# Optimization experiments

Hardware: AMD Instinct MI355X
Metric: run time of the kernel (lower is better)

The kernel has to match this reference:

```python
import jax, jax.numpy as jnp
import numpy as np

K = 3        # kernel size
PAD = 1      # padding
DG = 16      # deformable groups
MAXR = 10.0  # max_residue_magnitude


def _lrelu(x):
    return jnp.where(x >= 0, x, 0.1 * x)


def _conv3(x, w, b):
    y = jax.lax.conv_general_dilated(x, w, (1, 1), 'SAME',
                                     dimension_numbers=('NCHW', 'OIHW', 'NCHW'))
    return y + b[None, :, None, None]


def _deform_conv2d(x, offset, mask, weight, bias):
    # x: [B,Cin,H,W]; offset: [B,2*DG*K*K,H,W]; mask: [B,DG*K*K,H,W]
    B, Cin, H, W = x.shape
    Cout = weight.shape[0]
    G, Cg, K2 = DG, Cin // DG, K * K
    off = offset.reshape(B, G, K2, 2, H, W)
    dy, dx = off[:, :, :, 0], off[:, :, :, 1]
    ky = jnp.repeat(jnp.arange(K), K).astype(x.dtype)   # [K2]
    kx = jnp.tile(jnp.arange(K), K).astype(x.dtype)
    hh = jnp.arange(H, dtype=x.dtype)
    ww = jnp.arange(W, dtype=x.dtype)
    # sampling positions [B,G,K2,H,W]
    py = dy + ky[None, None, :, None, None] + hh[None, None, None, :, None] - PAD
    px = dx + kx[None, None, :, None, None] + ww[None, None, None, None, :] - PAD
    y0 = jnp.floor(py)
    x0 = jnp.floor(px)
    wy1 = py - y0
    wx1 = px - x0
    xf = x.reshape(B, G, Cg, H * W)

    def gather(yi, xi, wgt):
        valid = (yi >= 0) & (yi <= H - 1) & (xi >= 0) & (xi <= W - 1)
        idx = (jnp.clip(yi, 0, H - 1).astype(jnp.int32) * W
               + jnp.clip(xi, 0, W - 1).astype(jnp.int32)).reshape(B, G, -1)
        vals = jnp.take_along_axis(
            xf, jnp.broadcast_to(idx[:, :, None, :], (B, G, Cg, idx.shape[-1])), axis=3)
        vals = vals.reshape(B, G, Cg, K2, H, W)
        w = (wgt * valid.astype(x.dtype))[:, :, None]  # [B,G,1,K2,H,W]
        return vals * w

    s = (gather(y0, x0, (1 - wy1) * (1 - wx1))
         + gather(y0, x0 + 1, (1 - wy1) * wx1)
         + gather(y0 + 1, x0, wy1 * (1 - wx1))
         + gather(y0 + 1, x0 + 1, wy1 * wx1))
    s = s * mask.reshape(B, G, K2, H, W)[:, :, None]
    wr = weight.reshape(Cout, G, Cg, K2)
    out = jnp.einsum('ogck,bgckhw->bohw', wr, s)
    return out + bias[None, :, None, None]


def setup_inputs() -> dict:
    key = jax.random.key(0)
    ks = jax.random.split(key, 16)
    B, Cin, Cout, H, W = 4, 128, 64, 96, 96
    Coff = 3 * Cout + 4  # 196
    stdv = 1.0 / np.sqrt(Cin * K * K)
    inp = {
        'x': jax.random.normal(ks[0], (B, Cin, H, W), jnp.float32),
        'extra_feat': jax.random.normal(ks[1], (B, 3 * Cout, H, W), jnp.float32),
        'flow_1': jax.random.normal(ks[2], (B, 2, H, W), jnp.float32),
        'flow_2': jax.random.normal(ks[3], (B, 2, H, W), jnp.float32),
        'weight': jax.random.uniform(ks[4], (Cout, Cin, K, K), jnp.float32, -stdv, stdv),
        'bias': jax.random.normal(ks[5], (Cout,), jnp.float32) * 0.01,
        'ow0': jax.random.normal(ks[6], (Cout, Coff, K, K), jnp.float32) * 0.02,
        'ob0': jnp.zeros((Cout,), jnp.float32),
        'ow1': jax.random.normal(ks[7], (Cout, Cout, K, K), jnp.float32) * 0.02,
        'ob1': jnp.zeros((Cout,), jnp.float32),
        'ow2': jax.random.normal(ks[8], (Cout, Cout, K, K), jnp.float32) * 0.02,
        'ob2': jnp.zeros((Cout,), jnp.float32),
        'ow3': jax.random.normal(ks[9], (27 * DG, Cout, K, K), jnp.float32) * 0.01,
        'ob3': jnp.zeros((27 * DG,), jnp.float32),
    }
    return inp


def reference(x, extra_feat, flow_1, flow_2, weight, bias,
              ow0, ob0, ow1, ob1, ow2, ob2, ow3, ob3):
    feat = jnp.concatenate([extra_feat, flow_1, flow_2], axis=1)
    h = _lrelu(_conv3(feat, ow0, ob0))
    h = _lrelu(_conv3(h, ow1, ob1))
    h = _lrelu(_conv3(h, ow2, ob2))
    out = _conv3(h, ow3, ob3)
    o1, o2, m = jnp.split(out, 3, axis=1)
    offs = MAXR * jnp.tanh(jnp.concatenate([o1, o2], axis=1))
    off1, off2 = jnp.split(offs, 2, axis=1)
    off1 = off1 + jnp.tile(flow_1[:, ::-1], (1, off1.shape[1] // 2, 1, 1))
    off2 = off2 + jnp.tile(flow_2[:, ::-1], (1, off2.shape[1] // 2, 1, 1))
    offset = jnp.concatenate([off1, off2], axis=1)
    mask = jax.nn.sigmoid(m)
    return _deform_conv2d(x, offset, mask, weight, bias)
```

## Files before the change

### kernel.cpp

```cpp
#include <hip/hip_runtime.h>
#include <math.h>

#define HW 9216
#define Hh 96
#define Ww 96
#define PHW 9604

typedef __attribute__((ext_vector_type(8))) short bh8;
typedef __attribute__((ext_vector_type(4))) short bh4;
typedef __attribute__((ext_vector_type(4))) float f32x4;
typedef __attribute__((ext_vector_type(2))) float f32x2;
typedef __attribute__((ext_vector_type(4))) int i32x4;
union bh8i { bh8 v; i32x4 i; };

__device__ __forceinline__ short f2bf(float f) {
    union { float f; unsigned u; } v; v.f = f;
    unsigned r = v.u + 0x7FFFu + ((v.u >> 16) & 1u);
    return (short)(r >> 16);
}
__device__ __forceinline__ float bf2f(short s) {
    union { unsigned u; float f; } v; v.u = ((unsigned)(unsigned short)s) << 16;
    return v.f;
}
__device__ __forceinline__ float lo_bf(unsigned u) {
    union { unsigned u; float f; } v; v.u = u << 16; return v.f;
}
__device__ __forceinline__ float hi_bf(unsigned u) {
    union { unsigned u; float f; } v; v.u = u & 0xFFFF0000u; return v.f;
}
__device__ __forceinline__ int cvt_pk_bf16(float lo, float hi) {
    int r;
    asm("v_cvt_pk_bf16_f32 %0, %1, %2" : "=v"(r) : "v"(lo), "v"(hi));
    return r;
}

__global__ void prep_misc(short* __restrict__ xpad1, short* __restrict__ hpa,
                          short* __restrict__ hpb, short* __restrict__ xdp,
                          const float* __restrict__ ow0, const float* __restrict__ ow1,
                          const float* __restrict__ ow2, const float* __restrict__ ow3,
                          const float* __restrict__ wd,
                          short* __restrict__ wb0, short* __restrict__ wb1,
                          short* __restrict__ wb2, short* __restrict__ wb3,
                          short* __restrict__ wbd) {
    int i = blockIdx.x * 256 + threadIdx.x;
    const int z1 = 4 * 388 * 224, z2 = 4 * 388 * 64;
    if (i < z1 + 2 * z2) {
        short* p; int C;
        if (i < z1) { p = xpad1; C = 224; }
        else if (i < z1 + z2) { p = hpa; C = 64; i -= z1; }
        else { p = hpb; C = 64; i -= z1 + z2; }
        int c = i % C;
        int r = i / C;
        int b = r / 388, pid = r - b * 388;
        int row, col;
        if (pid < 98)       { row = 0;  col = pid; }
        else if (pid < 196) { row = 97; col = pid - 98; }
        else if (pid < 292) { row = pid - 196 + 1; col = 0; }
        else                { row = pid - 292 + 1; col = 97; }
        p[((size_t)b * PHW + row * 98 + col) * C + c] = 0;
        return;
    }
    i -= z1 + 2 * z2;
    const int zr = 4 * 16 * 388 * 8;
    if (i < zr) {
        int c8 = i & 7;
        int r = i >> 3;
        int pid = r % 388;
        int bg = r / 388;
        int row, col;
        if (pid < 98)       { row = 0;  col = pid; }
        else if (pid < 196) { row = 97; col = pid - 98; }
        else if (pid < 292) { row = pid - 196 + 1; col = 0; }
        else                { row = pid - 292 + 1; col = 97; }
        xdp[((size_t)bg * PHW + row * 98 + col) * 8 + c8] = 0;
        return;
    }
    i -= zr;
    const int n0 = 64 * 9 * 224, n1 = 64 * 9 * 64, n3 = 448 * 9 * 64, nd = 64 * 1152;
    if (i < n0) {
        int co = i / (9 * 224); int r = i - co * (9 * 224);
        int tap = r / 224, ci = r - tap * 224;
        wb0[i] = f2bf(ci < 196 ? ow0[(co * 196 + ci) * 9 + tap] : 0.f);
        return;
    }
    i -= n0;
    if (i < n1) {
        int co = i / (9 * 64); int r = i - co * (9 * 64);
        int tap = r / 64, ci = r - tap * 64;
        wb1[i] = f2bf(ow1[(co * 64 + ci) * 9 + tap]);
        return;
    }
    i -= n1;
    if (i < n1) {
        int co = i / (9 * 64); int r = i - co * (9 * 64);
        int tap = r / 64, ci = r - tap * 64;
        wb2[i] = f2bf(ow2[(co * 64 + ci) * 9 + tap]);
        return;
    }
    i -= n1;
    if (i < n3) {
        int co = i / (9 * 64); int r = i - co * (9 * 64);
        int tap = r / 64, ci = r - tap * 64;
        wb3[i] = f2bf(co < 432 ? ow3[(co * 64 + ci) * 9 + tap] : 0.f);
        return;
    }
    i -= n3;
    if (i < nd) {
        int slab = i >> 11, r = i & 2047;
        int co = r >> 5, k = r & 31;
        int gt = slab * 4 + (k >> 3), c8 = k & 7;
        int g = gt / 9, tap = gt - g * 9;
        wbd[i] = f2bf(wd[(co * 128 + g * 8 + c8) * 9 + tap]);
    }
}

__global__ void pack_all(const float* __restrict__ extra,
                         const float* __restrict__ f1,
                         const float* __restrict__ f2,
                         const float* __restrict__ x,
                         short* __restrict__ xp,
                         short* __restrict__ xdp) {
    __shared__ float t[32][33];
    const int tid = threadIdx.x, tx = tid & 31, ty = tid >> 5;
    const int pt = blockIdx.x, b = blockIdx.z;
    if (blockIdx.y < 7) {
        const int ct = blockIdx.y;
#pragma unroll
        for (int j = 0; j < 4; ++j) {
            int ch = ct * 32 + ty + j * 8;
            int p = pt * 32 + tx;
            float v = 0.f;
            if (ch < 192)      v = extra[(b * 192 + ch) * HW + p];
            else if (ch < 194) v = f1[(b * 2 + ch - 192) * HW + p];
            else if (ch < 196) v = f2[(b * 2 + ch - 194) * HW + p];
            t[ty + j * 8][tx] = v;
        }
        __syncthreads();
#pragma unroll
        for (int j = 0; j < 4; ++j) {
            int pr = ty + j * 8;
            int p = pt * 32 + pr;
            int r = p / 96, c = p - r * 96;
            xp[((size_t)b * PHW + (r + 1) * 98 + (c + 1)) * 224 + ct * 32 + tx] =
                f2bf(t[tx][pr]);
        }
    } else {
        const int ct = blockIdx.y - 7;
#pragma unroll
        for (int j = 0; j < 4; ++j) {
            int ch = ct * 32 + ty + j * 8;
            t[ty + j * 8][tx] = x[((size_t)b * 128 + ch) * HW + pt * 32 + tx];
        }
        __syncthreads();
        if (tid < 128) {
            int oct = tid >> 5, p = tid & 31;
            int g = ct * 4 + oct;
            int pix = pt * 32 + p;
            int r = pix / 96, c = pix - r * 96;
            bh8 v;
#pragma unroll
            for (int cc = 0; cc < 8; ++cc) v[cc] = f2bf(t[oct * 8 + cc][p]);
            *(bh8*)&xdp[(((size_t)b * 16 + g) * PHW + (r + 1) * 98 + (c + 1)) * 8] = v;
        }
    }
}

template<int CINP, int KCH>
__launch_bounds__(256)
__global__ void conv_mfma(const short* __restrict__ xp,
                          const short* __restrict__ wb,
                          const float* __restrict__ bias,
                          short* __restrict__ o1) {
    __shared__ __attribute__((aligned(16))) short smA[9 * 64 * 32];
    const int tid = threadIdx.x;
    const int lane = tid & 63, wv = tid >> 6;
    const int q = lane >> 4, l15 = lane & 15;
    const int b = blockIdx.y;
    const int pix0 = blockIdx.x * 64 + wv * 16;
    const int soh = pix0 / 96, sow = pix0 - (pix0 / 96) * 96;

    const short* bp = xp + ((size_t)b * PHW + soh * 98 + sow + l15) * CINP + q * 8;

    const int sco = tid >> 2, sqq = tid & 3;
    const short* wsrc = wb + (size_t)sco * (9 * CINP) + sqq * 8;

    f32x4 acc[4];
#pragma unroll
    for (int t = 0; t < 4; ++t) acc[t] = (f32x4){0.f, 0.f, 0.f, 0.f};

    for (int p = 0; p < KCH; ++p) {
        __syncthreads();
        bh8 wtmp[9];
#pragma unroll
        for (int tap = 0; tap < 9; ++tap)
            wtmp[tap] = *(const bh8*)(wsrc + tap * CINP + p * 32);
#pragma unroll
        for (int tap = 0; tap < 9; ++tap)
            *(bh8*)&smA[tap * 2048 + sco * 32 + sqq * 8] = wtmp[tap];
        __syncthreads();
#pragma unroll
        for (int tap = 0; tap < 9; ++tap) {
            const int ky = tap / 3, kx = tap - (tap / 3) * 3;
            bh8 bf = *(const bh8*)(bp + (ky * 98 + kx) * CINP + p * 32);
#pragma unroll
            for (int t = 0; t < 4; ++t) {
                bh8 af = *(const bh8*)&smA[tap * 2048 + (t * 16 + l15) * 32 + q * 8];
                acc[t] = __builtin_amdgcn_mfma_f32_16x16x32_bf16(af, bf, acc[t], 0, 0, 0);
            }
        }
    }

    size_t base = ((size_t)b * PHW + (soh + 1) * 98 + sow + l15 + 1) * 64;
#pragma unroll
    for (int t = 0; t < 4; ++t) {
        bh4 v4;
#pragma unroll
        for (int r = 0; r < 4; ++r) {
            int co = t * 16 + q * 4 + r;
            float v = acc[t][r] + bias[co];
            v = (v >= 0.f) ? v : 0.1f * v;
            v4[r] = f2bf(v);
        }
        *(bh4*)(o1 + base + t * 16 + q * 4) = v4;
    }
}

__launch_bounds__(256)
__global__ void conv4_mfma(const short* __restrict__ xp,
                           const short* __restrict__ wb,
                           const float* __restrict__ bias,
                           float* __restrict__ offp,
                           short* __restrict__ maskb,
                           const float* __restrict__ flow1,
                           const float* __restrict__ flow2) {
    __shared__ __attribute__((aligned(16))) short smA[9 * 64 * 32];
    const int tid = threadIdx.x;
    const int lane = tid & 63, wv = tid >> 6;
    const int q = lane >> 4, l15 = lane & 15;
    const int b = blockIdx.y;
    const int cob = blockIdx.z * 64;
    const int pix0 = blockIdx.x * 64 + wv * 16;
    const int soh = pix0 / 96, sow = pix0 - (pix0 / 96) * 96;

    const short* bp = xp + ((size_t)b * PHW + soh * 98 + sow + l15) * 64 + q * 8;

    const int sco = tid >> 2, sqq = tid & 3;
    const short* wsrc = wb + (size_t)(cob + sco) * 576 + sqq * 8;

    f32x4 acc[4];
#pragma unroll
    for (int t = 0; t < 4; ++t) acc[t] = (f32x4){0.f, 0.f, 0.f, 0.f};

    for (int p = 0; p < 2; ++p) {
        __syncthreads();
        bh8 wtmp[9];
#pragma unroll
        for (int tap = 0; tap < 9; ++tap)
            wtmp[tap] = *(const bh8*)(wsrc + tap * 64 + p * 32);
#pragma unroll
        for (int tap = 0; tap < 9; ++tap)
            *(bh8*)&smA[tap * 2048 + sco * 32 + sqq * 8] = wtmp[tap];
        __syncthreads();
#pragma unroll
        for (int tap = 0; tap < 9; ++tap) {
            const int ky = tap / 3, kx = tap - (tap / 3) * 3;
            bh8 bf = *(const bh8*)(bp + (ky * 98 + kx) * 64 + p * 32);
#pragma unroll
            for (int t = 0; t < 4; ++t) {
                bh8 af = *(const bh8*)&smA[tap * 2048 + (t * 16 + l15) * 32 + q * 8];
                acc[t] = __builtin_amdgcn_mfma_f32_16x16x32_bf16(af, bf, acc[t], 0, 0, 0);
            }
        }
    }

    const int pix = pix0 + l15;
#pragma unroll
    for (int t = 0; t < 4; ++t) {
        int cb0 = cob + t * 16 + q * 4;
        if (cb0 < 288) {
            const float* fl = (cb0 < 144) ? flow1 : flow2;
            float fe = fl[(b * 2 + 1) * HW + pix];
            float fo = fl[(b * 2) * HW + pix];
            float t0 = 10.f * tanhf(acc[t][0] + bias[cb0 + 0]) + fe;
            float t1 = 10.f * tanhf(acc[t][1] + bias[cb0 + 1]) + fo;
            float t2 = 10.f * tanhf(acc[t][2] + bias[cb0 + 2]) + fe;
            float t3 = 10.f * tanhf(acc[t][3] + bias[cb0 + 3]) + fo;
            size_t p0 = ((size_t)b * 144 + (cb0 >> 1)) * HW + pix;
            *(f32x2*)&offp[p0 * 2] = (f32x2){t0, t1};
            *(f32x2*)&offp[(p0 + HW) * 2] = (f32x2){t2, t3};
        } else {
#pragma unroll
            for (int r = 0; r < 4; ++r) {
                int chn = cb0 + r;
                if (chn < 432) {
                    float v = acc[t][r] + bias[chn];
                    maskb[((size_t)b * 144 + (chn - 288)) * HW + pix] =
                        f2bf(1.f / (1.f + expf(-v)));
                }
            }
        }
    }
}

#define BLEND_MFMA(C0, C1, C2, C3, WWv, CL)                                    \
    {                                                                          \
        const f32x2 W00 = (f32x2){(WWv)[0], (WWv)[0]};                         \
        const f32x2 W01 = (f32x2){(WWv)[1], (WWv)[1]};                         \
        const f32x2 W10 = (f32x2){(WWv)[2], (WWv)[2]};                         \
        const f32x2 W11 = (f32x2){(WWv)[3], (WWv)[3]};                         \
        bh8i bf;                                                               \
        _Pragma("unroll")                                                      \
        for (int k = 0; k < 4; ++k) {                                          \
            unsigned u00 = (unsigned)(C0).i[k], u01 = (unsigned)(C1).i[k];     \
            unsigned u10 = (unsigned)(C2).i[k], u11 = (unsigned)(C3).i[k];     \
            f32x2 p00 = (f32x2){lo_bf(u00), hi_bf(u00)};                       \
            f32x2 p01 = (f32x2){lo_bf(u01), hi_bf(u01)};                       \
            f32x2 p10 = (f32x2){lo_bf(u10), hi_bf(u10)};                       \
            f32x2 p11 = (f32x2){lo_bf(u11), hi_bf(u11)};                       \
            f32x2 s = p00 * W00 + p01 * W01 + p10 * W10 + p11 * W11;           \
            bf.i[k] = cvt_pk_bf16(s[0], s[1]);                                 \
        }                                                                      \
        _Pragma("unroll")                                                      \
        for (int t = 0; t < 4; ++t) {                                          \
            bh8 af = *(const bh8*)&smW[(CL) * 2048 + (t * 16 + l15) * 32 + q * 8]; \
            acc[t] = __builtin_amdgcn_mfma_f32_16x16x32_bf16(af, bf.v, acc[t], 0, 0, 0); \
        }                                                                      \
    }

__launch_bounds__(256)
__global__ void deform_mfma(const short* __restrict__ xdp,
                            const float* __restrict__ offp,
                            const short* __restrict__ maskb,
                            const short* __restrict__ wbd,
                            const float* __restrict__ bias,
                            float* __restrict__ out) {
    __shared__ __attribute__((aligned(16))) short smW[3 * 2048];
    const int tid = threadIdx.x;
    const int lane = tid & 63, wv = tid >> 6;
    const int q = lane >> 4, l15 = lane & 15;
    const int blk = blockIdx.x;
    const int xs = blk & 7, idx = blk >> 3;
    const int b = xs >> 1, gh = xs & 1;
    const int pixw = idx * 64 + wv * 16 + l15;
    const int h = pixw / 96, w = pixw - (pixw / 96) * 96;

    const float* opp = offp + ((size_t)(b * 144 + gh * 72) * HW + pixw) * 2;
    const short* mp  = maskb + (size_t)(b * 144 + gh * 72) * HW + pixw;
    const short* xb  = xdp + (size_t)b * 16 * PHW * 8;
    const short* wsrc = wbd + (size_t)(gh * 18) * 2048 + tid * 8;

    f32x4 acc[4];
#pragma unroll
    for (int t = 0; t < 4; ++t) acc[t] = (f32x4){0.f, 0.f, 0.f, 0.f};

    f32x2 dc[3]; float mc[3];
#pragma unroll
    for (int cl = 0; cl < 3; ++cl) {
        int lt = cl * 4 + q;
        dc[cl] = *(const f32x2*)(opp + (size_t)lt * HW * 2);
        mc[cl] = bf2f(mp[(size_t)lt * HW]);
    }

    for (int r = 0; r < 6; ++r) {
        __syncthreads();
        bh8 st0 = *(const bh8*)(wsrc + (r * 3 + 0) * 2048);
        bh8 st1 = *(const bh8*)(wsrc + (r * 3 + 1) * 2048);
        bh8 st2 = *(const bh8*)(wsrc + (r * 3 + 2) * 2048);
        *(bh8*)&smW[0 * 2048 + tid * 8] = st0;
        *(bh8*)&smW[1 * 2048 + tid * 8] = st1;
        *(bh8*)&smW[2 * 2048 + tid * 8] = st2;
        __syncthreads();

        f32x2 dn[3]; float mn[3];
        if (r < 5) {
#pragma unroll
            for (int cl = 0; cl < 3; ++cl) {
                int lt = ((r + 1) * 3 + cl) * 4 + q;
                dn[cl] = *(const f32x2*)(opp + (size_t)lt * HW * 2);
                mn[cl] = bf2f(mp[(size_t)lt * HW]);
            }
        }

        int soff[3]; f32x4 ww[3];
#pragma unroll
        for (int cl = 0; cl < 3; ++cl) {
            int gt = gh * 72 + (r * 3 + cl) * 4 + q;
            int g = gt / 9, tap = gt - g * 9;
            float py = dc[cl][0] + (float)(tap / 3) + (float)h - 1.f;
            float px = dc[cl][1] + (float)(tap - (tap / 3) * 3) + (float)w - 1.f;
            py = fminf(fmaxf(py, -1.f), 96.f);
            px = fminf(fmaxf(px, -1.f), 96.f);
            float y0f = floorf(py), x0f = floorf(px);
            float wy1 = py - y0f, wx1 = px - x0f;
            float wy0 = 1.f - wy1, wx0 = 1.f - wx1;
            int yp = (int)y0f + 1, xq = (int)x0f + 1;
            soff[cl] = (g * PHW + yp * 98 + xq) * 8;
            float m = mc[cl];
            ww[cl] = (f32x4){wy0 * wx0 * m, wy0 * wx1 * m, wy1 * wx0 * m, wy1 * wx1 * m};
        }

        bh8i a0, a1, a2, a3, b0, b1, b2, b3;
        {
            const short* p = xb + soff[0];
            a0.v = *(const bh8*)(p);          a1.v = *(const bh8*)(p + 8);
            a2.v = *(const bh8*)(p + 98 * 8); a3.v = *(const bh8*)(p + 99 * 8);
        }
        {
            const short* p = xb + soff[1];
            b0.v = *(const bh8*)(p);          b1.v = *(const bh8*)(p + 8);
            b2.v = *(const bh8*)(p + 98 * 8); b3.v = *(const bh8*)(p + 99 * 8);
        }
        BLEND_MFMA(a0, a1, a2, a3, ww[0], 0);
        {
            const short* p = xb + soff[2];
            a0.v = *(const bh8*)(p);          a1.v = *(const bh8*)(p + 8);
            a2.v = *(const bh8*)(p + 98 * 8); a3.v = *(const bh8*)(p + 99 * 8);
        }
        BLEND_MFMA(b0, b1, b2, b3, ww[1], 1);
        BLEND_MFMA(a0, a1, a2, a3, ww[2], 2);

        if (r < 5) {
#pragma unroll
            for (int cl = 0; cl < 3; ++cl) { dc[cl] = dn[cl]; mc[cl] = mn[cl]; }
        }
    }

#pragma unroll
    for (int t = 0; t < 4; ++t)
#pragma unroll
        for (int rr = 0; rr < 4; ++rr) {
            int co = t * 16 + q * 4 + rr;
            float v = acc[t][rr];
            if (gh == 0) v += bias[co];
            atomicAdd(&out[((size_t)b * 64 + co) * HW + pixw], v);
        }
}

extern "C" void kernel_launch(void* const* d_in, const int* in_sizes, int n_in,
                              void* d_out, int out_size, void* d_ws, size_t ws_size,
                              hipStream_t stream) {
    const float* x      = (const float*)d_in[0];
    const float* extra  = (const float*)d_in[1];
    const float* flow1  = (const float*)d_in[2];
    const float* flow2  = (const float*)d_in[3];
    const float* weight = (const float*)d_in[4];
    const float* bias   = (const float*)d_in[5];
    const float* ow0    = (const float*)d_in[6];
    const float* ob0    = (const float*)d_in[7];
    const float* ow1    = (const float*)d_in[8];
    const float* ob1    = (const float*)d_in[9];
    const float* ow2    = (const float*)d_in[10];
    const float* ob2    = (const float*)d_in[11];
    const float* ow3    = (const float*)d_in[12];
    const float* ob3    = (const float*)d_in[13];
    float* out = (float*)d_out;

    char* wsb = (char*)d_ws;
    short* xpad1 = (short*)wsb;   wsb += (size_t)4 * PHW * 224 * 2;
    short* hpa   = (short*)wsb;   wsb += (size_t)4 * PHW * 64 * 2;
    short* hpb   = (short*)wsb;   wsb += (size_t)4 * PHW * 64 * 2;
    float* offpair = (float*)wsb; wsb += (size_t)4 * 144 * HW * 2 * 4;
    short* maskbuf = (short*)wsb; wsb += (size_t)4 * 144 * HW * 2;
    short* xdp     = (short*)wsb; wsb += (size_t)4 * 16 * PHW * 8 * 2 + 32;
    short* wb0     = (short*)wsb; wsb += 64 * 9 * 224 * 2;
    short* wb1     = (short*)wsb; wsb += 64 * 9 * 64 * 2;
    short* wb2     = (short*)wsb; wsb += 64 * 9 * 64 * 2;
    short* wb3     = (short*)wsb; wsb += 448 * 9 * 64 * 2;
    short* wbd     = (short*)wsb;

    hipMemsetAsync(out, 0, out_size, stream);

    const int prep_total = 546304 + 198656 + 534528;
    prep_misc<<<dim3((prep_total + 255) / 256), 256, 0, stream>>>(
        xpad1, hpa, hpb, xdp, ow0, ow1, ow2, ow3, weight,
        wb0, wb1, wb2, wb3, wbd);
    pack_all<<<dim3(288, 11, 4), 256, 0, stream>>>(extra, flow1, flow2, x, xpad1, xdp);

    conv_mfma<224, 7><<<dim3(144, 4), 256, 0, stream>>>(xpad1, wb0, ob0, hpa);
    conv_mfma<64, 2><<<dim3(144, 4), 256, 0, stream>>>(hpa, wb1, ob1, hpb);
    conv_mfma<64, 2><<<dim3(144, 4), 256, 0, stream>>>(hpb, wb2, ob2, hpa);
    conv4_mfma<<<dim3(144, 4, 7), 256, 0, stream>>>(hpa, wb3, ob3, offpair,
                                                    maskbuf, flow1, flow2);
    deform_mfma<<<dim3(1152), 256, 0, stream>>>(xdp, offpair, maskbuf, wbd, bias, out);
}
```

Measured before the change: 282.4 us.

## Pre-swizzle conv4 weights into MFMA fragment order and drop LDS staging

The conv4 weight packing now writes the weights directly in the per-lane MFMA A-fragment order, indexed by cout block, input half, tap, tile and lane. The conv4 kernel then loads its A fragments straight from global memory with coalesced 16-byte reads. This removes the shared-memory staging buffer and both __syncthreads per input half. It also adds an occupancy hint of 6 in launch_bounds, since the kernel no longer uses LDS. The trade-off is that every wave re-reads the weights through the cache instead of sharing them from LDS, which adds global or L2 traffic.

```diff
diff --git a/kernel.cpp b/kernel.cpp
--- a/kernel.cpp
+++ b/kernel.cpp
@@ -99,8 +99,15 @@
     }
     i -= n1;
     if (i < n3) {
-        int co = i / (9 * 64); int r = i - co * (9 * 64);
-        int tap = r / 64, ci = r - tap * 64;
+        int c8 = i & 7;
+        int r = i >> 3;
+        int lane = r & 63; r >>= 6;
+        int t = r & 3; r >>= 2;
+        int tap = r % 9; r /= 9;
+        int p = r & 1;
+        int cob = r >> 1;
+        int co = cob * 64 + t * 16 + (lane & 15);
+        int ci = p * 32 + (lane >> 4) * 8 + c8;
         wb3[i] = f2bf(co < 432 ? ow3[(co * 64 + ci) * 9 + tap] : 0.f);
         return;
     }
@@ -225,7 +232,7 @@
     }
 }
 
-__launch_bounds__(256)
+__launch_bounds__(256, 6)
 __global__ void conv4_mfma(const short* __restrict__ xp,
                            const short* __restrict__ wb,
                            const float* __restrict__ bias,
@@ -233,7 +240,6 @@
                            short* __restrict__ maskb,
                            const float* __restrict__ flow1,
                            const float* __restrict__ flow2) {
-    __shared__ __attribute__((aligned(16))) short smA[9 * 64 * 32];
     const int tid = threadIdx.x;
     const int lane = tid & 63, wv = tid >> 6;
     const int q = lane >> 4, l15 = lane & 15;
@@ -242,32 +248,24 @@
     const int pix0 = blockIdx.x * 64 + wv * 16;
     const int soh = pix0 / 96, sow = pix0 - (pix0 / 96) * 96;
 
-    const short* bp = xp + ((size_t)b * PHW + soh * 98 + sow + l15) * 64 + q * 8;
-
-    const int sco = tid >> 2, sqq = tid & 3;
-    const short* wsrc = wb + (size_t)(cob + sco) * 576 + sqq * 8;
+    const short* wbase = wb + (size_t)blockIdx.z * (2 * 9 * 4 * 64 * 8) + lane * 8;
 
     f32x4 acc[4];
 #pragma unroll
     for (int t = 0; t < 4; ++t) acc[t] = (f32x4){0.f, 0.f, 0.f, 0.f};
 
+#pragma unroll
     for (int p = 0; p < 2; ++p) {
-        __syncthreads();
-        bh8 wtmp[9];
-#pragma unroll
-        for (int tap = 0; tap < 9; ++tap)
-            wtmp[tap] = *(const bh8*)(wsrc + tap * 64 + p * 32);
-#pragma unroll
-        for (int tap = 0; tap < 9; ++tap)
-            *(bh8*)&smA[tap * 2048 + sco * 32 + sqq * 8] = wtmp[tap];
-        __syncthreads();
+        const short* bp = xp + ((size_t)b * PHW + soh * 98 + sow + l15) * 64
+                          + q * 8 + p * 32;
+        const short* wp = wbase + p * (9 * 4 * 64 * 8);
 #pragma unroll
         for (int tap = 0; tap < 9; ++tap) {
             const int ky = tap / 3, kx = tap - (tap / 3) * 3;
-            bh8 bf = *(const bh8*)(bp + (ky * 98 + kx) * 64 + p * 32);
+            bh8 bf = *(const bh8*)(bp + (ky * 98 + kx) * 64);
 #pragma unroll
             for (int t = 0; t < 4; ++t) {
-                bh8 af = *(const bh8*)&smA[tap * 2048 + (t * 16 + l15) * 32 + q * 8];
+                bh8 af = *(const bh8*)(wp + (tap * 4 + t) * 512);
                 acc[t] = __builtin_amdgcn_mfma_f32_16x16x32_bf16(af, bf, acc[t], 0, 0, 0);
             }
         }
```

Result: slower. 296.8 us (+5.1%).
